# Performance work log

Measured on AMD Instinct MI355X. Metric: run time of the kernel, lower is better.

Reference implementation:

```python
import jax, jax.numpy as jnp
import numpy as np
import math

B, C, SEG, SEGLEN, K, GROUPS, WG = 8, 256, 40, 200, 10, 32, 4
L4 = SEGLEN // 4            # 50 temporal slots per segment
N = SEG * L4                # 2000 total points
WIDTH = GROUPS * WG         # 128 bottleneck width


def build_neighbor_idx(seg_lens):
    """Exact numpy replication of torch get_temporal_graph's neighbor-list loop.
    Returns flat (into B*N rows) neighbor indices of shape (B, N, 3)."""
    seg_lens = np.asarray(seg_lens)
    Bn, S = seg_lens.shape
    nb = np.zeros((Bn, S * L4, 3), dtype=np.int64)
    for i in range(Bn):
        last_valid = 0
        skip_seg = 0
        base = i * S * L4
        for j in range(S):
            valid = math.ceil(seg_lens[i, j] / 4.0)
            for k in range(L4):
                idx = j * L4 + k
                if k < valid:
                    nb[i, idx] = [base + last_valid, base + idx, base + idx]
                    last_valid = idx
                    if k == 0 and j != 0:
                        nb[i, skip_seg, 2] = base + idx
                    if k == valid - 1:
                        skip_seg = idx
                    else:
                        nb[i, idx, 2] = base + idx + 1
                else:
                    nb[i, idx] = [base + idx] * 3
    return nb


def conv1x1(x, W, b):
    # x: (B, Cin, N, T), W: (Cout, Cin)
    return jnp.einsum('bcnt,oc->bont', x, W) + b[None, :, None, None]


def grouped_1x3(x, W, b):
    # x: (B, WIDTH, N, 3), W: (WIDTH, WIDTH//GROUPS, 3); valid conv -> T_out = 1
    Bn, _, Nn, _ = x.shape
    xg = x.reshape(Bn, GROUPS, WIDTH // GROUPS, Nn, 3)
    Wg = W.reshape(GROUPS, WIDTH // GROUPS, WIDTH // GROUPS, 3)
    y = jnp.einsum('bgcnt,goct->bgon', xg, Wg)
    return y.reshape(Bn, WIDTH, Nn, 1) + b[None, :, None, None]


def grouped_1x1(x, W, b):
    # x: (B, WIDTH, N, T), W: (WIDTH, WIDTH//GROUPS)
    Bn, _, Nn, T = x.shape
    xg = x.reshape(Bn, GROUPS, WIDTH // GROUPS, Nn, T)
    Wg = W.reshape(GROUPS, WIDTH // GROUPS, WIDTH // GROUPS)
    y = jnp.einsum('bgcnt,goc->bgont', xg, Wg)
    return y.reshape(Bn, WIDTH, Nn, T) + b[None, :, None, None]


def setup_inputs() -> dict:
    key = jax.random.key(0)
    ks = jax.random.split(key, 10)
    s = 0.05
    x = jax.random.normal(ks[0], (B, C, N), dtype=jnp.float32)
    seg_lens = jax.random.randint(ks[1], (B, SEG), 0, 201)
    neighbor_idx = jnp.asarray(build_neighbor_idx(np.asarray(seg_lens)))
    return dict(
        x=x, seg_lens=seg_lens, neighbor_idx=neighbor_idx,
        tW1=jax.random.normal(ks[2], (WIDTH, C), jnp.float32) * s,
        tb1=jnp.zeros((WIDTH,), jnp.float32),
        tW2=jax.random.normal(ks[3], (WIDTH, WIDTH // GROUPS, 3), jnp.float32) * s,
        tb2=jnp.zeros((WIDTH,), jnp.float32),
        tW3=jax.random.normal(ks[4], (C, WIDTH), jnp.float32) * s,
        tb3=jnp.zeros((C,), jnp.float32),
        sW1=jax.random.normal(ks[5], (WIDTH, 2 * C), jnp.float32) * s,
        sb1=jnp.zeros((WIDTH,), jnp.float32),
        sW2=jax.random.normal(ks[6], (WIDTH, WIDTH // GROUPS), jnp.float32) * s,
        sb2=jnp.zeros((WIDTH,), jnp.float32),
        sW3=jax.random.normal(ks[7], (C, WIDTH), jnp.float32) * s,
        sb3=jnp.zeros((C,), jnp.float32),
    )


def reference(x, seg_lens, neighbor_idx, tW1, tb1, tW2, tb2, tW3, tb3,
              sW1, sb1, sW2, sb2, sW3, sb3):
    relu = jax.nn.relu
    B_, C_, N_ = x.shape
    flat = x.transpose(0, 2, 1).reshape(B_ * N_, C_)  # (B*N, C)

    # --- temporal branch: gather 3 temporal-graph neighbors -> (B, C, N, 3) ---
    tg = flat[neighbor_idx.reshape(-1)].reshape(B_, N_, 3, C_).transpose(0, 3, 1, 2)
    h = relu(conv1x1(tg, tW1, tb1))
    h = relu(grouped_1x3(h, tW2, tb2))
    tout = conv1x1(h, tW3, tb3).max(axis=-1)  # (B, C, N)

    # --- semantic branch: kNN graph feature (style=1) ---
    xx = jnp.sum(x * x, axis=1)                       # (B, N)
    inner = jnp.einsum('bci,bcj->bij', x, x)          # (B, N, N)
    pd = 2.0 * inner - xx[:, None, :] - xx[:, :, None]  # negative sq. distances
    _, idx = jax.lax.top_k(pd, K)                     # (B, N, K)
    base = (jnp.arange(B_) * N_)[:, None, None]
    nbr = flat[(idx + base).reshape(-1)].reshape(B_, N_, K, C_)
    center = jnp.broadcast_to(x.transpose(0, 2, 1)[:, :, None, :], (B_, N_, K, C_))
    xf = jnp.concatenate([nbr, center], axis=3).transpose(0, 3, 1, 2)  # (B, 2C, N, K)
    g = relu(conv1x1(xf, sW1, sb1))
    g = relu(grouped_1x1(g, sW2, sb2))
    sout = conv1x1(g, sW3, sb3).max(axis=-1)  # (B, C, N)

    return relu(tout + x + sout)
```

## Files before the change

### kernel.cpp

```cpp
#include <hip/hip_runtime.h>

#define NPTS 2000
#define NBATCH 8
#define NC 256
#define NW 128
#define NK 10
#define NROWS (NBATCH * NPTS)
#define JPAD 2048
#define PL2 (JPAD * 32)

typedef _Float16 f16x8 __attribute__((ext_vector_type(8)));
typedef _Float16 f16x4 __attribute__((ext_vector_type(4)));
typedef float f32x4 __attribute__((ext_vector_type(4)));

__device__ __forceinline__ float dot4(float4 a, float4 b) {
    return a.x*b.x + a.y*b.y + a.z*b.z + a.w*b.w;
}
__device__ __forceinline__ float4 relu4(float4 a) {
    return make_float4(fmaxf(a.x,0.f), fmaxf(a.y,0.f), fmaxf(a.z,0.f), fmaxf(a.w,0.f));
}
__device__ __forceinline__ float4 add4(float4 a, float4 b) {
    return make_float4(a.x+b.x, a.y+b.y, a.z+b.z, a.w+b.w);
}

__device__ __forceinline__ void ins10(float d, int j, float* vals, int* idxs) {
    if (d > vals[9]) {
        float v = d; int id = j;
        #pragma unroll
        for (int s = 0; s < 10; ++s) {
            if (v > vals[s]) {
                float tv = vals[s]; vals[s] = v; v = tv;
                int   ti = idxs[s]; idxs[s] = id; id = ti;
            }
        }
    }
}

__global__ __launch_bounds__(256) void k_prep(
    const float* __restrict__ x, _Float16* __restrict__ xb,
    float* __restrict__ xx)
{
    __shared__ float T[64][259];
    __shared__ float Pp[64][4];
    const int t  = threadIdx.x;
    const int b  = blockIdx.x >> 5;
    const int n0 = (blockIdx.x & 31) * 64;

    #pragma unroll
    for (int p = 0; p < 64; ++p) {
        const int idx = p*256 + t;
        const int c = idx >> 6, nl = idx & 63;
        T[nl][c] = x[((size_t)b*NC + c)*NPTS + min(n0 + nl, NPTS-1)];
    }
    __syncthreads();

    const int row = t & 63, q = t >> 6;
    const int gr  = n0 + row;
    const bool ok = gr < NPTS;
    float ss = 0.f;
    #pragma unroll
    for (int u = 0; u < 2; ++u) {
        const int kc = 2*q + u;
        const size_t bh = ((size_t)(b*8 + kc)*2    )*PL2 + (size_t)gr*32;
        const size_t bl = ((size_t)(b*8 + kc)*2 + 1)*PL2 + (size_t)gr*32;
        #pragma unroll
        for (int g = 0; g < 4; ++g) {
            f16x8 vh, vl;
            #pragma unroll
            for (int e = 0; e < 8; ++e) {
                const float f = ok ? T[row][kc*32 + g*8 + e] : 0.f;
                ss = fmaf(f, f, ss);
                const _Float16 h = (_Float16)f;
                vh[e] = h;
                vl[e] = (_Float16)(f - (float)h);
            }
            *(f16x8*)&xb[bh + g*8] = vh;
            *(f16x8*)&xb[bl + g*8] = vl;
        }
    }
    Pp[row][q] = ss;
    __syncthreads();
    if (t < 64 && n0 + t < NPTS)
        xx[(size_t)b*NPTS + n0 + t] = Pp[t][0] + Pp[t][1] + Pp[t][2] + Pp[t][3];
}

__global__ __launch_bounds__(256) void k_wprep(const float* __restrict__ a,
                                               _Float16* __restrict__ o, int n)
{
    const int i = (blockIdx.x*256 + threadIdx.x)*4;
    if (i < n) {
        const float4 v = *(const float4*)&a[i];
        f16x4 h = {(_Float16)v.x, (_Float16)v.y, (_Float16)v.z, (_Float16)v.w};
        *(f16x4*)&o[i] = h;
    }
}

__global__ __launch_bounds__(256) void k_rowgemm(
    const float* __restrict__ x,
    const float* __restrict__ tW1, const float* __restrict__ tb1,
    const float* __restrict__ sW1, const float* __restrict__ sb1,
    float* __restrict__ T1r, float* __restrict__ P, float* __restrict__ Q)
{
    __shared__ float Xs[32][34];
    __shared__ float Ws[32][132];
    const int t  = threadIdx.x;
    const int r0 = blockIdx.x * 32;
    const int sel = blockIdx.y;
    const int jq = t & 15,  iq = t >> 4;
    const int j0 = jq * 8,  i0 = iq * 2;

    float acc[2][8];
    #pragma unroll
    for (int a = 0; a < 2; ++a)
        #pragma unroll
        for (int q = 0; q < 8; ++q) acc[a][q] = 0.f;

    const int li = t & 31;
    const int lk = t >> 5;
    const int rl = r0 + li;
    const int lb = rl / NPTS, ln = rl % NPTS;

    for (int c0 = 0; c0 < NC; c0 += 32) {
        #pragma unroll
        for (int p = 0; p < 4; ++p) {
            int kk = lk + p * 8;
            Xs[kk][li] = x[((size_t)lb * NC + c0 + kk) * NPTS + ln];
        }
        #pragma unroll
        for (int jj = 0; jj < 16; ++jj) {
            int j = jj * 8 + lk;
            int c = c0 + li;
            float w;
            if (sel == 0)      w = tW1[j * NC + c];
            else if (sel == 1) w = sW1[j * (2*NC) + c];
            else               w = sW1[j * (2*NC) + NC + c];
            Ws[li][j] = w;
        }
        __syncthreads();
        #pragma unroll 8
        for (int kk = 0; kk < 32; ++kk) {
            const float2 xv = *(const float2*)&Xs[kk][i0];
            const float4 w0 = *(const float4*)&Ws[kk][j0];
            const float4 w1 = *(const float4*)&Ws[kk][j0 + 4];
            float w[8] = {w0.x,w0.y,w0.z,w0.w,w1.x,w1.y,w1.z,w1.w};
            #pragma unroll
            for (int q = 0; q < 8; ++q) {
                acc[0][q] = fmaf(xv.x, w[q], acc[0][q]);
                acc[1][q] = fmaf(xv.y, w[q], acc[1][q]);
            }
        }
        __syncthreads();
    }

    #pragma unroll
    for (int a = 0; a < 2; ++a) {
        const int r = r0 + i0 + a;
        float o[8];
        #pragma unroll
        for (int q = 0; q < 8; ++q) {
            float v = acc[a][q];
            if (sel == 0)      { v += tb1[j0+q]; v = fmaxf(v, 0.f); }
            else if (sel == 2) { v += sb1[j0+q]; }
            o[q] = v;
        }
        float* dst = (sel==0 ? T1r : (sel==1 ? P : Q)) + (size_t)r * NW + j0;
        *(float4*)dst       = make_float4(o[0],o[1],o[2],o[3]);
        *(float4*)(dst + 4) = make_float4(o[4],o[5],o[6],o[7]);
    }
}

__global__ __launch_bounds__(256, 3) void k_topk(
    const _Float16* __restrict__ xb, const float* __restrict__ xx,
    float* __restrict__ pval, int* __restrict__ pidx)
{
    __shared__ __align__(16) char smem[20480];
    float* xxs = (float*)smem;

    const int t    = threadIdx.x;
    const int b    = blockIdx.x & 7;
    const int ig   = (blockIdx.x >> 3) & 31;
    const int jh   = blockIdx.x >> 8;
    const int i0   = ig * 64;
    const int lane = t & 63;
    const int w    = t >> 6;
    const int lr   = lane & 15, rg = lane >> 4;
    const size_t bbase = (size_t)b * 16 * PL2;
    const int jbase  = jh * 672;
    const int ntiles = (jh == 2) ? 41 : 42;

    {
        const int ncnt = ntiles * 16;
        for (int idx = t; idx < ncnt; idx += 256)
            xxs[idx] = xx[(size_t)b*NPTS + jbase + idx];
    }

    f16x8 bh[8], bl[8];
    {
        const int i = min(i0 + w*16 + lr, NPTS - 1);
        #pragma unroll
        for (int kc = 0; kc < 8; ++kc) {
            const size_t ph = bbase + (size_t)(kc*2)*PL2 + (size_t)i*32 + rg*8;
            bh[kc] = *(const f16x8*)&xb[ph];
            bl[kc] = *(const f16x8*)&xb[ph + PL2];
        }
    }

    float vals[10]; int idxs[10];
    #pragma unroll
    for (int s = 0; s < 10; ++s) { vals[s] = -3.0e38f; idxs[s] = 0x7fffffff; }

    __syncthreads();

    for (int jt = 0; jt < ntiles; ++jt) {
        const int j0 = jbase + jt*16;
        const size_t ja = (size_t)(j0 + lr)*32 + rg*8;

        f32x4 acc = {0.f,0.f,0.f,0.f};
        #pragma unroll
        for (int h = 0; h < 2; ++h) {
            f16x8 ah[4], al[4];
            #pragma unroll
            for (int k4 = 0; k4 < 4; ++k4) {
                const int kc = h*4 + k4;
                ah[k4] = *(const f16x8*)&xb[bbase + (size_t)(kc*2    )*PL2 + ja];
                al[k4] = *(const f16x8*)&xb[bbase + (size_t)(kc*2 + 1)*PL2 + ja];
            }
            #pragma unroll
            for (int k4 = 0; k4 < 4; ++k4) {
                const int kc = h*4 + k4;
                acc = __builtin_amdgcn_mfma_f32_16x16x32_f16(ah[k4], bh[kc], acc, 0,0,0);
                acc = __builtin_amdgcn_mfma_f32_16x16x32_f16(ah[k4], bl[kc], acc, 0,0,0);
                acc = __builtin_amdgcn_mfma_f32_16x16x32_f16(al[k4], bh[kc], acc, 0,0,0);
            }
        }

        {
            const int jr = jt*16 + rg*4;
            const f32x4 xv = *(const f32x4*)&xxs[jr];
            const float d0 = 2.f*acc[0] - xv[0];
            const float d1 = 2.f*acc[1] - xv[1];
            const float d2 = 2.f*acc[2] - xv[2];
            const float d3 = 2.f*acc[3] - xv[3];
            const float mx = fmaxf(fmaxf(d0, d1), fmaxf(d2, d3));
            if (mx > vals[9]) {
                const int jg = j0 + rg*4;
                ins10(d0, jg,     vals, idxs);
                ins10(d1, jg + 1, vals, idxs);
                ins10(d2, jg + 2, vals, idxs);
                ins10(d3, jg + 3, vals, idxs);
            }
        }
    }

    __syncthreads();
    float* mval = (float*)smem;
    int*   midx = (int*)(smem + 10240);
    {
        const int g = w*16 + lr;
        #pragma unroll
        for (int s = 0; s < 10; ++s) {
            mval[(g*4 + rg)*10 + s] = vals[s];
            midx[(g*4 + rg)*10 + s] = idxs[s];
        }
    }
    __syncthreads();
    if (t < 128) {
        const int g = t >> 1, pr = t & 1;
        float* va = &mval[(g*4 + pr)*10];     int* ia = &midx[(g*4 + pr)*10];
        const float* vb = &mval[(g*4 + pr + 2)*10]; const int* ib = &midx[(g*4 + pr + 2)*10];
        float ov[10]; int oi[10]; int pa = 0, pb = 0;
        #pragma unroll
        for (int s = 0; s < 10; ++s) {
            const float A = va[pa], Bv = vb[pb];
            const int  Ai = ia[pa], Bi = ib[pb];
            const bool ta = (A > Bv) || (A == Bv && Ai < Bi);
            ov[s] = ta ? A : Bv; oi[s] = ta ? Ai : Bi;
            pa += ta ? 1 : 0; pb += ta ? 0 : 1;
        }
        #pragma unroll
        for (int s = 0; s < 10; ++s) { va[s] = ov[s]; ia[s] = oi[s]; }
    }
    __syncthreads();
    if (t < 64) {
        const int g = t;
        const int i = i0 + g;
        if (i < NPTS) {
            const float* va = &mval[(g*4 + 0)*10]; const int* ia = &midx[(g*4 + 0)*10];
            const float* vb = &mval[(g*4 + 1)*10]; const int* ib = &midx[(g*4 + 1)*10];
            float* ov = &pval[((size_t)(b*NPTS + i)*3 + jh)*10];
            int*   oi = &pidx[((size_t)(b*NPTS + i)*3 + jh)*10];
            int pa = 0, pb = 0;
            #pragma unroll
            for (int s = 0; s < 10; ++s) {
                const float A = va[pa], Bv = vb[pb];
                const int  Ai = ia[pa], Bi = ib[pb];
                const bool ta = (A > Bv) || (A == Bv && Ai < Bi);
                ov[s] = ta ? A : Bv; oi[s] = ta ? Ai : Bi;
                pa += ta ? 1 : 0; pb += ta ? 0 : 1;
            }
        }
    }
}

__global__ __launch_bounds__(256) void k_tkmerge(
    const float* __restrict__ pval, const int* __restrict__ pidx,
    int* __restrict__ tk)
{
    const int r = blockIdx.x*256 + threadIdx.x;
    if (r >= NROWS) return;
    const float* v  = &pval[(size_t)r*30];
    const int*   ix = &pidx[(size_t)r*30];
    const int base = (r / NPTS) * NPTS;
    int* op = &tk[(size_t)r*NK];
    int p0 = 0, p1 = 0, p2 = 0;
    #pragma unroll
    for (int s = 0; s < NK; ++s) {
        float bv = -3.4e38f; int bi = 0x7fffffff; int bl = 0;
        {
            const float vv = v[p0];       const int ii = ix[p0];
            if (vv > bv || (vv == bv && ii < bi)) { bv = vv; bi = ii; bl = 0; }
        }
        {
            const float vv = v[10 + p1];  const int ii = ix[10 + p1];
            if (vv > bv || (vv == bv && ii < bi)) { bv = vv; bi = ii; bl = 1; }
        }
        {
            const float vv = v[20 + p2];  const int ii = ix[20 + p2];
            if (vv > bv || (vv == bv && ii < bi)) { bv = vv; bi = ii; bl = 2; }
        }
        p0 += (bl == 0); p1 += (bl == 1); p2 += (bl == 2);
        op[s] = base + bi;
    }
}

#define AST 136
__global__ __launch_bounds__(256, 2) void k_fused(
    const float* __restrict__ x,
    const int* __restrict__ nb, const int* __restrict__ tk,
    const float* __restrict__ T1r, const float* __restrict__ P, const float* __restrict__ Q,
    const float* __restrict__ tW2, const float* __restrict__ tb2,
    const float* __restrict__ sW2, const float* __restrict__ sb2,
    const _Float16* __restrict__ wt3h, const _Float16* __restrict__ ws3h,
    const float* __restrict__ tb3, const float* __restrict__ sb3,
    float* __restrict__ out)
{
    __shared__ __align__(16) _Float16 A16[144*AST];
    __shared__ float Ssm[8][260];
    __shared__ float Zr[8][260];

    const int t  = threadIdx.x;
    const int r0 = blockIdx.x * 8;
    const int bb = r0 / NPTS;
    const int n0 = r0 % NPTS;

    {
        const float4 z4 = make_float4(0.f,0.f,0.f,0.f);
        float4* p4 = (float4*)A16;
        #pragma unroll
        for (int i = 0; i < 10; ++i) {
            const int idx = t + i*256;
            if (idx < 2448) p4[idx] = z4;
        }
    }
    __syncthreads();

    {
        const int o    = t & 127;
        const int half = t >> 7;
        const int g4   = o & ~3;

        const float4 f0 = *(const float4*)&tW2[o*12];
        const float4 f1 = *(const float4*)&tW2[o*12 + 4];
        const float4 f2 = *(const float4*)&tW2[o*12 + 8];
        const float4 wt0 = make_float4(f0.x, f0.w, f1.z, f2.y);
        const float4 wt1 = make_float4(f0.y, f1.x, f1.w, f2.z);
        const float4 wt2 = make_float4(f0.z, f1.y, f2.x, f2.w);
        const float4 wsw = *(const float4*)&sW2[o*4];
        const float tb2o = tb2[o], sb2o = sb2[o];

        #pragma unroll
        for (int ptl = 0; ptl < 4; ++ptl) {
            const int pt = half*4 + ptl;
            const int r  = r0 + pt;
            const int nb0 = nb[r*3+0], nb1 = nb[r*3+1], nb2 = nb[r*3+2];
            int ki[NK];
            #pragma unroll
            for (int k = 0; k < NK; ++k) ki[k] = tk[r*NK + k];
            const float4 h0 = *(const float4*)&T1r[(size_t)nb0*NW + g4];
            const float4 h1 = *(const float4*)&T1r[(size_t)nb1*NW + g4];
            const float4 h2 = *(const float4*)&T1r[(size_t)nb2*NW + g4];
            const float4 qf = *(const float4*)&Q[(size_t)r*NW + g4];
            float4 pf[NK];
            #pragma unroll
            for (int k = 0; k < NK; ++k) pf[k] = *(const float4*)&P[(size_t)ki[k]*NW + g4];

            const float z = tb2o + dot4(wt0,h0) + dot4(wt1,h1) + dot4(wt2,h2);
            A16[(128 + pt)*AST + o] = (_Float16)fmaxf(z, 0.f);
            #pragma unroll
            for (int k = 0; k < NK; ++k) {
                const float4 g1 = relu4(add4(pf[k], qf));
                A16[(pt*16 + k)*AST + o] = (_Float16)fmaxf(dot4(wsw, g1) + sb2o, 0.f);
            }
        }
    }
    __syncthreads();

    const int lane = t & 63, w = t >> 6;
    const int lr = lane & 15, lg = lane >> 4;
    const int n0w = w * 64;

    f32x4 accG[8][4] = {};
    f32x4 accZ[4] = {};

    #pragma unroll
    for (int kt = 0; kt < 4; ++kt) {
        const int ko = kt*32 + lg*8;
        f16x8 bs[4], bt[4];
        #pragma unroll
        for (int nt = 0; nt < 4; ++nt) {
            const int n = n0w + nt*16 + lr;
            bs[nt] = *(const f16x8*)&ws3h[n*NW + ko];
            bt[nt] = *(const f16x8*)&wt3h[n*NW + ko];
        }
        #pragma unroll
        for (int mt = 0; mt < 8; ++mt) {
            const f16x8 a = *(const f16x8*)&A16[(mt*16 + lr)*AST + ko];
            #pragma unroll
            for (int nt = 0; nt < 4; ++nt)
                accG[mt][nt] = __builtin_amdgcn_mfma_f32_16x16x32_f16(a, bs[nt], accG[mt][nt], 0,0,0);
        }
        const f16x8 az = *(const f16x8*)&A16[(128 + lr)*AST + ko];
        #pragma unroll
        for (int nt = 0; nt < 4; ++nt)
            accZ[nt] = __builtin_amdgcn_mfma_f32_16x16x32_f16(az, bt[nt], accZ[nt], 0,0,0);
    }

    const int rg = lg;
    #pragma unroll
    for (int mt = 0; mt < 8; ++mt) {
        #pragma unroll
        for (int nt = 0; nt < 4; ++nt) {
            float v;
            if (rg < 2)       v = fmaxf(fmaxf(accG[mt][nt][0], accG[mt][nt][1]),
                                        fmaxf(accG[mt][nt][2], accG[mt][nt][3]));
            else if (rg == 2) v = fmaxf(accG[mt][nt][0], accG[mt][nt][1]);
            else              v = -3.0e38f;
            v = fmaxf(v, __shfl_xor(v, 16));
            v = fmaxf(v, __shfl_xor(v, 32));
            if (lane < 16) Ssm[mt][n0w + nt*16 + lane] = v;
        }
    }
    #pragma unroll
    for (int nt = 0; nt < 4; ++nt) {
        #pragma unroll
        for (int q = 0; q < 4; ++q) {
            if (rg < 2) Zr[rg*4 + q][n0w + nt*16 + lr] = accZ[nt][q];
        }
    }
    __syncthreads();

    {
        const int c = t;
        const float tb = tb3[c], sb = sb3[c];
        const size_t go = ((size_t)bb*NC + c)*NPTS + n0;
        const float4 xv0 = *(const float4*)&x[go];
        const float4 xv1 = *(const float4*)&x[go + 4];
        const float xr[8] = {xv0.x,xv0.y,xv0.z,xv0.w, xv1.x,xv1.y,xv1.z,xv1.w};
        float ov[8];
        #pragma unroll
        for (int p = 0; p < 8; ++p)
            ov[p] = fmaxf(Zr[p][c] + tb + Ssm[p][c] + sb + xr[p], 0.f);
        *(float4*)&out[go]     = make_float4(ov[0],ov[1],ov[2],ov[3]);
        *(float4*)&out[go + 4] = make_float4(ov[4],ov[5],ov[6],ov[7]);
    }
}

extern "C" void kernel_launch(void* const* d_in, const int* in_sizes, int n_in,
                              void* d_out, int out_size, void* d_ws, size_t ws_size,
                              hipStream_t stream) {
    (void)in_sizes; (void)n_in; (void)out_size; (void)ws_size;
    const float* x   = (const float*)d_in[0];
    const int*   nb  = (const int*)d_in[2];
    const float* tW1 = (const float*)d_in[3];
    const float* tb1 = (const float*)d_in[4];
    const float* tW2 = (const float*)d_in[5];
    const float* tb2 = (const float*)d_in[6];
    const float* tW3 = (const float*)d_in[7];
    const float* tb3 = (const float*)d_in[8];
    const float* sW1 = (const float*)d_in[9];
    const float* sb1 = (const float*)d_in[10];
    const float* sW2 = (const float*)d_in[11];
    const float* sb2 = (const float*)d_in[12];
    const float* sW3 = (const float*)d_in[13];
    const float* sb3 = (const float*)d_in[14];
    float* out = (float*)d_out;

    float* ws  = (float*)d_ws;
    float* T1r  = ws;
    float* P    = ws + 2048000;
    float* Q    = ws + 4096000;
    float* xxp  = ws + 6144000;
    int*   tk   = (int*)(ws + 6160000);
    float* pval = ws + 6320000;
    int*   pidx = (int*)(ws + 6800000);
    _Float16* xb   = (_Float16*)(ws + 7280000);
    _Float16* wt3h = xb + (size_t)NBATCH * 16 * PL2;
    _Float16* ws3h = wt3h + NC * NW;

    k_prep<<<NBATCH * 32, 256, 0, stream>>>(x, xb, xxp);
    k_wprep<<<32, 256, 0, stream>>>(tW3, wt3h, NC * NW);
    k_wprep<<<32, 256, 0, stream>>>(sW3, ws3h, NC * NW);
    k_rowgemm<<<dim3(NROWS / 32, 3), 256, 0, stream>>>(x, tW1, tb1, sW1, sb1, T1r, P, Q);
    k_topk<<<768, 256, 0, stream>>>(xb, xxp, pval, pidx);
    k_tkmerge<<<(NROWS + 255) / 256, 256, 0, stream>>>(pval, pidx, tk);
    k_fused<<<NROWS / 8, 256, 0, stream>>>(x, nb, tk, T1r, P, Q,
                                           tW2, tb2, sW2, sb2, wt3h, ws3h, tb3, sb3, out);
}
```

Measured before the change: 458.5 us.

## Interleave fp16 split layout, MFMA first-layer GEMM, double-buffered top-k in halves

Moves the split-fp16 x buffer from plane-major to row-major (hi/lo interleaved per row). The fp32 first-layer row GEMM becomes an MFMA kernel that uses a concatenated fp16 weight matrix and only the hi part of the weights. The kNN top-k kernel now splits the j range into two halves instead of three, with register double-buffered tile loads, and the merge kernel is simplified to a two-way merge. Together these aim to cut the first-layer GEMM cost and memory stalls in top-k, at the cost of fp16 rounding of W1 and higher register pressure in top-k (occupancy bound lowered to 2).

Result: faster. 392.7 us (-14.3%).

```diff
diff --git a/kernel.cpp b/kernel.cpp
--- a/kernel.cpp
+++ b/kernel.cpp
@@ -7,7 +7,6 @@
 #define NK 10
 #define NROWS (NBATCH * NPTS)
 #define JPAD 2048
-#define PL2 (JPAD * 32)
 
 typedef _Float16 f16x8 __attribute__((ext_vector_type(8)));
 typedef _Float16 f16x4 __attribute__((ext_vector_type(4)));
@@ -57,12 +56,11 @@
     const int row = t & 63, q = t >> 6;
     const int gr  = n0 + row;
     const bool ok = gr < NPTS;
+    const size_t rb = ((size_t)b*JPAD + gr) * 512;
     float ss = 0.f;
     #pragma unroll
     for (int u = 0; u < 2; ++u) {
         const int kc = 2*q + u;
-        const size_t bh = ((size_t)(b*8 + kc)*2    )*PL2 + (size_t)gr*32;
-        const size_t bl = ((size_t)(b*8 + kc)*2 + 1)*PL2 + (size_t)gr*32;
         #pragma unroll
         for (int g = 0; g < 4; ++g) {
             f16x8 vh, vl;
@@ -74,8 +72,8 @@
                 vh[e] = h;
                 vl[e] = (_Float16)(f - (float)h);
             }
-            *(f16x8*)&xb[bh + g*8] = vh;
-            *(f16x8*)&xb[bl + g*8] = vl;
+            *(f16x8*)&xb[rb + (kc*2    )*32 + g*8] = vh;
+            *(f16x8*)&xb[rb + (kc*2 + 1)*32 + g*8] = vl;
         }
     }
     Pp[row][q] = ss;
@@ -95,81 +93,62 @@
     }
 }
 
-__global__ __launch_bounds__(256) void k_rowgemm(
-    const float* __restrict__ x,
-    const float* __restrict__ tW1, const float* __restrict__ tb1,
-    const float* __restrict__ sW1, const float* __restrict__ sb1,
+__global__ __launch_bounds__(256) void k_wcat(
+    const float* __restrict__ tW1, const float* __restrict__ sW1,
+    _Float16* __restrict__ whcat)
+{
+    const int idx = blockIdx.x*256 + threadIdx.x;
+    const int n = idx >> 8, k = idx & 255;
+    float v;
+    if (n < 128)      v = tW1[n*256 + k];
+    else if (n < 256) v = sW1[(n-128)*512 + k];
+    else              v = sW1[(n-256)*512 + 256 + k];
+    whcat[idx] = (_Float16)v;
+}
+
+__global__ __launch_bounds__(256) void k_rowmm(
+    const _Float16* __restrict__ xb, const _Float16* __restrict__ whcat,
+    const float* __restrict__ tb1, const float* __restrict__ sb1,
     float* __restrict__ T1r, float* __restrict__ P, float* __restrict__ Q)
 {
-    __shared__ float Xs[32][34];
-    __shared__ float Ws[32][132];
-    const int t  = threadIdx.x;
-    const int r0 = blockIdx.x * 32;
-    const int sel = blockIdx.y;
-    const int jq = t & 15,  iq = t >> 4;
-    const int j0 = jq * 8,  i0 = iq * 2;
-
-    float acc[2][8];
-    #pragma unroll
-    for (int a = 0; a < 2; ++a)
-        #pragma unroll
-        for (int q = 0; q < 8; ++q) acc[a][q] = 0.f;
-
-    const int li = t & 31;
-    const int lk = t >> 5;
-    const int rl = r0 + li;
-    const int lb = rl / NPTS, ln = rl % NPTS;
-
-    for (int c0 = 0; c0 < NC; c0 += 32) {
-        #pragma unroll
-        for (int p = 0; p < 4; ++p) {
-            int kk = lk + p * 8;
-            Xs[kk][li] = x[((size_t)lb * NC + c0 + kk) * NPTS + ln];
-        }
-        #pragma unroll
-        for (int jj = 0; jj < 16; ++jj) {
-            int j = jj * 8 + lk;
-            int c = c0 + li;
-            float w;
-            if (sel == 0)      w = tW1[j * NC + c];
-            else if (sel == 1) w = sW1[j * (2*NC) + c];
-            else               w = sW1[j * (2*NC) + NC + c];
-            Ws[li][j] = w;
-        }
-        __syncthreads();
-        #pragma unroll 8
-        for (int kk = 0; kk < 32; ++kk) {
-            const float2 xv = *(const float2*)&Xs[kk][i0];
-            const float4 w0 = *(const float4*)&Ws[kk][j0];
-            const float4 w1 = *(const float4*)&Ws[kk][j0 + 4];
-            float w[8] = {w0.x,w0.y,w0.z,w0.w,w1.x,w1.y,w1.z,w1.w};
-            #pragma unroll
-            for (int q = 0; q < 8; ++q) {
-                acc[0][q] = fmaf(xv.x, w[q], acc[0][q]);
-                acc[1][q] = fmaf(xv.y, w[q], acc[1][q]);
-            }
-        }
-        __syncthreads();
-    }
-
-    #pragma unroll
-    for (int a = 0; a < 2; ++a) {
-        const int r = r0 + i0 + a;
-        float o[8];
-        #pragma unroll
-        for (int q = 0; q < 8; ++q) {
-            float v = acc[a][q];
-            if (sel == 0)      { v += tb1[j0+q]; v = fmaxf(v, 0.f); }
-            else if (sel == 2) { v += sb1[j0+q]; }
-            o[q] = v;
-        }
-        float* dst = (sel==0 ? T1r : (sel==1 ? P : Q)) + (size_t)r * NW + j0;
-        *(float4*)dst       = make_float4(o[0],o[1],o[2],o[3]);
-        *(float4*)(dst + 4) = make_float4(o[4],o[5],o[6],o[7]);
-    }
-}
-
-__global__ __launch_bounds__(256, 3) void k_topk(
+    const int t = threadIdx.x, lane = t & 63, w = t >> 6;
+    const int lr = lane & 15, rg = lane >> 4;
+    const int r0 = blockIdx.x * 16;
+    const int b  = r0 / NPTS, jr = r0 % NPTS;
+
+    f16x8 ah[8], al[8];
+    const size_t rb = ((size_t)b*JPAD + jr + lr) * 512 + rg*8;
+    #pragma unroll
+    for (int kc = 0; kc < 8; ++kc) {
+        ah[kc] = *(const f16x8*)&xb[rb + kc*64];
+        al[kc] = *(const f16x8*)&xb[rb + kc*64 + 32];
+    }
+
+    #pragma unroll
+    for (int nt = 0; nt < 6; ++nt) {
+        const int n0 = (w*6 + nt) * 16;
+        f32x4 acc = {0.f,0.f,0.f,0.f};
+        #pragma unroll
+        for (int kc = 0; kc < 8; ++kc) {
+            const f16x8 bw = *(const f16x8*)&whcat[(size_t)(n0 + lr)*256 + kc*32 + rg*8];
+            acc = __builtin_amdgcn_mfma_f32_16x16x32_f16(ah[kc], bw, acc, 0,0,0);
+            acc = __builtin_amdgcn_mfma_f32_16x16x32_f16(al[kc], bw, acc, 0,0,0);
+        }
+        const int n = n0 + lr;
+        float bias; bool dorelu; float* dst;
+        if (n < 128)      { bias = tb1[n];     dorelu = true;  dst = T1r + (size_t)r0*NW + n; }
+        else if (n < 256) { bias = 0.f;        dorelu = false; dst = P   + (size_t)r0*NW + (n-128); }
+        else              { bias = sb1[n-256]; dorelu = false; dst = Q   + (size_t)r0*NW + (n-256); }
+        #pragma unroll
+        for (int q = 0; q < 4; ++q) {
+            float v = acc[q] + bias;
+            if (dorelu) v = fmaxf(v, 0.f);
+            dst[(size_t)(rg*4 + q)*NW] = v;
+        }
+    }
+}
+
+__global__ __launch_bounds__(256, 2) void k_topk(
     const _Float16* __restrict__ xb, const float* __restrict__ xx,
     float* __restrict__ pval, int* __restrict__ pidx)
 {
@@ -184,24 +163,24 @@
     const int lane = t & 63;
     const int w    = t >> 6;
     const int lr   = lane & 15, rg = lane >> 4;
-    const size_t bbase = (size_t)b * 16 * PL2;
-    const int jbase  = jh * 672;
-    const int ntiles = (jh == 2) ? 41 : 42;
-
-    {
-        const int ncnt = ntiles * 16;
-        for (int idx = t; idx < ncnt; idx += 256)
-            xxs[idx] = xx[(size_t)b*NPTS + jbase + idx];
+    const size_t bj = (size_t)b * JPAD;
+    const int tile0  = jh * 63;
+    const int ntiles = jh ? 62 : 63;
+
+    {
+        const int cnt = ntiles * 16;
+        for (int idx = t; idx < cnt; idx += 256)
+            xxs[idx] = xx[(size_t)b*NPTS + tile0*16 + idx];
     }
 
     f16x8 bh[8], bl[8];
     {
         const int i = min(i0 + w*16 + lr, NPTS - 1);
+        const size_t rb = (bj + i) * 512 + rg*8;
         #pragma unroll
         for (int kc = 0; kc < 8; ++kc) {
-            const size_t ph = bbase + (size_t)(kc*2)*PL2 + (size_t)i*32 + rg*8;
-            bh[kc] = *(const f16x8*)&xb[ph];
-            bl[kc] = *(const f16x8*)&xb[ph + PL2];
+            bh[kc] = *(const f16x8*)&xb[rb + kc*64];
+            bl[kc] = *(const f16x8*)&xb[rb + kc*64 + 32];
         }
     }
 
@@ -211,46 +190,48 @@
 
     __syncthreads();
 
-    for (int jt = 0; jt < ntiles; ++jt) {
-        const int j0 = jbase + jt*16;
-        const size_t ja = (size_t)(j0 + lr)*32 + rg*8;
-
-        f32x4 acc = {0.f,0.f,0.f,0.f};
-        #pragma unroll
-        for (int h = 0; h < 2; ++h) {
-            f16x8 ah[4], al[4];
-            #pragma unroll
-            for (int k4 = 0; k4 < 4; ++k4) {
-                const int kc = h*4 + k4;
-                ah[k4] = *(const f16x8*)&xb[bbase + (size_t)(kc*2    )*PL2 + ja];
-                al[k4] = *(const f16x8*)&xb[bbase + (size_t)(kc*2 + 1)*PL2 + ja];
-            }
-            #pragma unroll
-            for (int k4 = 0; k4 < 4; ++k4) {
-                const int kc = h*4 + k4;
-                acc = __builtin_amdgcn_mfma_f32_16x16x32_f16(ah[k4], bh[kc], acc, 0,0,0);
-                acc = __builtin_amdgcn_mfma_f32_16x16x32_f16(ah[k4], bl[kc], acc, 0,0,0);
-                acc = __builtin_amdgcn_mfma_f32_16x16x32_f16(al[k4], bh[kc], acc, 0,0,0);
-            }
-        }
-
-        {
-            const int jr = jt*16 + rg*4;
-            const f32x4 xv = *(const f32x4*)&xxs[jr];
-            const float d0 = 2.f*acc[0] - xv[0];
-            const float d1 = 2.f*acc[1] - xv[1];
-            const float d2 = 2.f*acc[2] - xv[2];
-            const float d3 = 2.f*acc[3] - xv[3];
-            const float mx = fmaxf(fmaxf(d0, d1), fmaxf(d2, d3));
-            if (mx > vals[9]) {
-                const int jg = j0 + rg*4;
-                ins10(d0, jg,     vals, idxs);
-                ins10(d1, jg + 1, vals, idxs);
-                ins10(d2, jg + 2, vals, idxs);
-                ins10(d3, jg + 3, vals, idxs);
-            }
-        }
-    }
+    f16x8 RA[16], RB[16];
+    const size_t lbase = (bj + lr) * 512 + rg*8;
+
+#define LOADT(R, tt) { \
+    const size_t a_ = lbase + (size_t)(tile0 + (tt)) * 8192; \
+    _Pragma("unroll") \
+    for (int p = 0; p < 16; ++p) R[p] = *(const f16x8*)&xb[a_ + p*32]; }
+
+#define COMPUTE(R, tt) { \
+    f32x4 acc = {0.f,0.f,0.f,0.f}; \
+    _Pragma("unroll") \
+    for (int kc = 0; kc < 8; ++kc) { \
+        acc = __builtin_amdgcn_mfma_f32_16x16x32_f16(R[kc*2],   bh[kc], acc, 0,0,0); \
+        acc = __builtin_amdgcn_mfma_f32_16x16x32_f16(R[kc*2],   bl[kc], acc, 0,0,0); \
+        acc = __builtin_amdgcn_mfma_f32_16x16x32_f16(R[kc*2+1], bh[kc], acc, 0,0,0); \
+    } \
+    const int jr_ = (tt)*16 + rg*4; \
+    const f32x4 xv_ = *(const f32x4*)&xxs[jr_]; \
+    const float d0_ = 2.f*acc[0] - xv_[0]; \
+    const float d1_ = 2.f*acc[1] - xv_[1]; \
+    const float d2_ = 2.f*acc[2] - xv_[2]; \
+    const float d3_ = 2.f*acc[3] - xv_[3]; \
+    if (fmaxf(fmaxf(d0_,d1_), fmaxf(d2_,d3_)) > vals[9]) { \
+        const int jg_ = (tile0 + (tt))*16 + rg*4; \
+        ins10(d0_, jg_,     vals, idxs); \
+        ins10(d1_, jg_ + 1, vals, idxs); \
+        ins10(d2_, jg_ + 2, vals, idxs); \
+        ins10(d3_, jg_ + 3, vals, idxs); } }
+
+    LOADT(RA, 0)
+    int jt = 0;
+    while (jt + 2 <= ntiles) {
+        LOADT(RB, jt + 1)
+        COMPUTE(RA, jt)
+        if (jt + 2 < ntiles) LOADT(RA, jt + 2)
+        COMPUTE(RB, jt + 1)
+        jt += 2;
+    }
+    if (jt < ntiles) COMPUTE(RA, jt)
+
+#undef LOADT
+#undef COMPUTE
 
     __syncthreads();
     float* mval = (float*)smem;
@@ -287,8 +268,8 @@
         if (i < NPTS) {
             const float* va = &mval[(g*4 + 0)*10]; const int* ia = &midx[(g*4 + 0)*10];
             const float* vb = &mval[(g*4 + 1)*10]; const int* ib = &midx[(g*4 + 1)*10];
-            float* ov = &pval[((size_t)(b*NPTS + i)*3 + jh)*10];
-            int*   oi = &pidx[((size_t)(b*NPTS + i)*3 + jh)*10];
+            float* ov = &pval[((size_t)(b*NPTS + i)*2 + jh)*10];
+            int*   oi = &pidx[((size_t)(b*NPTS + i)*2 + jh)*10];
             int pa = 0, pb = 0;
             #pragma unroll
             for (int s = 0; s < 10; ++s) {
@@ -308,28 +289,20 @@
 {
     const int r = blockIdx.x*256 + threadIdx.x;
     if (r >= NROWS) return;
-    const float* v  = &pval[(size_t)r*30];
-    const int*   ix = &pidx[(size_t)r*30];
+    const float* va = &pval[(size_t)r*20];
+    const int*   ia = &pidx[(size_t)r*20];
+    const float* vb = va + 10;
+    const int*   ib = ia + 10;
     const int base = (r / NPTS) * NPTS;
     int* op = &tk[(size_t)r*NK];
-    int p0 = 0, p1 = 0, p2 = 0;
+    int pa = 0, pb = 0;
     #pragma unroll
     for (int s = 0; s < NK; ++s) {
-        float bv = -3.4e38f; int bi = 0x7fffffff; int bl = 0;
-        {
-            const float vv = v[p0];       const int ii = ix[p0];
-            if (vv > bv || (vv == bv && ii < bi)) { bv = vv; bi = ii; bl = 0; }
-        }
-        {
-            const float vv = v[10 + p1];  const int ii = ix[10 + p1];
-            if (vv > bv || (vv == bv && ii < bi)) { bv = vv; bi = ii; bl = 1; }
-        }
-        {
-            const float vv = v[20 + p2];  const int ii = ix[20 + p2];
-            if (vv > bv || (vv == bv && ii < bi)) { bv = vv; bi = ii; bl = 2; }
-        }
-        p0 += (bl == 0); p1 += (bl == 1); p2 += (bl == 2);
-        op[s] = base + bi;
+        const float A = va[pa], Bv = vb[pb];
+        const int  Ai = ia[pa], Bi = ib[pb];
+        const bool ta = (A > Bv) || (A == Bv && Ai < Bi);
+        op[s] = base + (ta ? Ai : Bi);
+        pa += ta ? 1 : 0; pb += ta ? 0 : 1;
     }
 }
 
@@ -502,16 +475,18 @@
     float* xxp  = ws + 6144000;
     int*   tk   = (int*)(ws + 6160000);
     float* pval = ws + 6320000;
-    int*   pidx = (int*)(ws + 6800000);
-    _Float16* xb   = (_Float16*)(ws + 7280000);
-    _Float16* wt3h = xb + (size_t)NBATCH * 16 * PL2;
-    _Float16* ws3h = wt3h + NC * NW;
+    int*   pidx = (int*)(ws + 6640000);
+    _Float16* xb    = (_Float16*)(ws + 6960000);
+    _Float16* whcat = xb + (size_t)NBATCH * JPAD * 512;
+    _Float16* wt3h  = whcat + 384 * 256;
+    _Float16* ws3h  = wt3h + NC * NW;
 
     k_prep<<<NBATCH * 32, 256, 0, stream>>>(x, xb, xxp);
+    k_wcat<<<384, 256, 0, stream>>>(tW1, sW1, whcat);
     k_wprep<<<32, 256, 0, stream>>>(tW3, wt3h, NC * NW);
     k_wprep<<<32, 256, 0, stream>>>(sW3, ws3h, NC * NW);
-    k_rowgemm<<<dim3(NROWS / 32, 3), 256, 0, stream>>>(x, tW1, tb1, sW1, sb1, T1r, P, Q);
-    k_topk<<<768, 256, 0, stream>>>(xb, xxp, pval, pidx);
+    k_rowmm<<<NROWS / 16, 256, 0, stream>>>(xb, whcat, tb1, sb1, T1r, P, Q);
+    k_topk<<<512, 256, 0, stream>>>(xb, xxp, pval, pidx);
     k_tkmerge<<<(NROWS + 255) / 256, 256, 0, stream>>>(pval, pidx, tk);
     k_fused<<<NROWS / 8, 256, 0, stream>>>(x, nb, tk, T1r, P, Q,
                                            tW2, tb2, sW2, sb2, wt3h, ws3h, tb3, sb3, out);
```
